# Kernel tuning notes

Measured on AMD Instinct MI355X. Metric: run time of the kernel, lower is better.

## Reference

```python
import jax, jax.numpy as jnp
import numpy as np

CTRL, WORD, MEM, D_IN = 256, 128, 128, 64
B, T = 512, 512
EPS = 1e-6


def setup_inputs() -> dict:
    key = jax.random.key(0)
    ks = jax.random.split(key, 16)
    rs = np.random.RandomState(0)

    data = jax.random.normal(ks[0], (T, B, D_IN), dtype=jnp.float32)

    # ragged lengths -> packed-style batch_sizes (descending, batch_sizes[0]=B)
    lengths = rs.randint(T // 2, T + 1, size=B)
    batch_sizes = jnp.asarray((lengths[None, :] > np.arange(T)[:, None]).sum(1),
                              dtype=jnp.int32)  # [T]
    unsort_idxs = jnp.asarray(rs.permutation(B), dtype=jnp.int32)

    sc = 0.02
    p = lambda k, sh: sc * jax.random.normal(k, sh, dtype=jnp.float32)
    return {
        "data": data,
        "batch_sizes": batch_sizes,
        "unsort_idxs": unsort_idxs,
        # GRU controller: input = D_IN + WORD, hidden = CTRL
        "W_ih": p(ks[1], (3 * CTRL, D_IN + WORD)),
        "b_ih": jnp.zeros((3 * CTRL,), jnp.float32),
        "W_hh": p(ks[2], (3 * CTRL, CTRL)),
        "b_hh": jnp.zeros((3 * CTRL,), jnp.float32),
        # memory head projections (from ctrl_out)
        "W_key": p(ks[3], (WORD, CTRL)), "b_key": jnp.zeros((WORD,), jnp.float32),
        "W_beta": p(ks[4], (1, CTRL)), "b_beta": jnp.zeros((1,), jnp.float32),
        "W_erase": p(ks[5], (WORD, CTRL)), "b_erase": jnp.zeros((WORD,), jnp.float32),
        "W_add": p(ks[6], (WORD, CTRL)), "b_add": jnp.zeros((WORD,), jnp.float32),
        # learned initial memory, shared across batch
        "M0": p(ks[7], (MEM, WORD)),
    }


def _gru(x, h, W_ih, b_ih, W_hh, b_hh):
    gi = x @ W_ih.T + b_ih          # [b, 3*CTRL]
    gh = h @ W_hh.T + b_hh
    ir, iz, inn = jnp.split(gi, 3, axis=-1)
    hr, hz, hn = jnp.split(gh, 3, axis=-1)
    r = jax.nn.sigmoid(ir + hr)
    z = jax.nn.sigmoid(iz + hz)
    n = jnp.tanh(inn + r * hn)
    return (1.0 - z) * n + z * h


def _memory(ctrl, M, W_key, b_key, W_beta, b_beta, W_erase, b_erase, W_add, b_add):
    # content addressing
    k = jnp.tanh(ctrl @ W_key.T + b_key)                       # [b, WORD]
    beta = jax.nn.softplus(ctrl @ W_beta.T + b_beta)           # [b, 1]
    Mn = M / (jnp.linalg.norm(M, axis=-1, keepdims=True) + EPS)
    kn = k / (jnp.linalg.norm(k, axis=-1, keepdims=True) + EPS)
    cos = jnp.einsum('bmw,bw->bm', Mn, kn)                     # [b, MEM]
    w = jax.nn.softmax(beta * cos, axis=-1)                    # [b, MEM]
    read = jnp.einsum('bm,bmw->bw', w, M)                      # [b, WORD]
    # erase/add write
    e = jax.nn.sigmoid(ctrl @ W_erase.T + b_erase)             # [b, WORD]
    a = ctrl @ W_add.T + b_add                                 # [b, WORD]
    M_new = M * (1.0 - w[:, :, None] * e[:, None, :]) + w[:, :, None] * a[:, None, :]
    return read, M_new


def reference(data, batch_sizes, unsort_idxs,
              W_ih, b_ih, W_hh, b_hh,
              W_key, b_key, W_beta, b_beta,
              W_erase, b_erase, W_add, b_add, M0):
    row = jnp.arange(B)

    def step(carry, inp):
        ctrl, read, M = carry
        x_t, size = inp
        active = (row < size)[:, None]                          # [B,1]
        ctrl_in = jnp.concatenate((x_t, read), axis=1)          # [B, D_IN+WORD]
        ctrl_new = _gru(ctrl_in, ctrl, W_ih, b_ih, W_hh, b_hh)
        read_new, M_new = _memory(ctrl_new, M, W_key, b_key, W_beta, b_beta,
                                  W_erase, b_erase, W_add, b_add)
        # inactive rows keep their final state (packed-batch semantics)
        ctrl = jnp.where(active, ctrl_new, ctrl)
        read = jnp.where(active, read_new, read)
        M = jnp.where(active[:, :, None], M_new, M)
        return (ctrl, read, M), None

    init = (jnp.zeros((B, CTRL), data.dtype),
            jnp.zeros((B, WORD), data.dtype),
            jnp.broadcast_to(M0, (B, MEM, WORD)))
    (ctrl, read, _), _ = jax.lax.scan(step, init, (data, batch_sizes))
    return ctrl[unsort_idxs], read[unsort_idxs]
```

## Files before the change

kernel.cpp:

```cpp
#include <hip/hip_runtime.h>
#include <math.h>

#define NB 512
#define NT 512
#define NCTRL 256
#define NWORD 128
#define NMEM 128
#define NDIN 64
#define NACT 448
#define EPSF 1e-6f

#define H_WA   0
#define H_WNI  229376
#define H_WNH  278528
#define H_WH   344064
#define H_TOTAL 475136
#define B_BA   0
#define B_BNI  512
#define B_BNH  768
#define B_BH   1024
#define B_TOTAL 1536
#define WS_BYTES (H_TOTAL * 2 + B_TOTAL * 4)

typedef _Float16 h2 __attribute__((ext_vector_type(2)));
typedef _Float16 h8 __attribute__((ext_vector_type(8)));
union H8 { h8 v; h2 d[4]; };

__device__ __forceinline__ float sigf(float x) { return 1.0f / (1.0f + expf(-x)); }
__device__ __forceinline__ float softplusf(float x) {
    return (x > 15.0f) ? x : log1pf(expf(x));
}
__device__ __forceinline__ float fdot2(h2 a, h2 b, float c) {
#if __has_builtin(__builtin_amdgcn_fdot2)
    return __builtin_amdgcn_fdot2(a, b, c, false);
#else
    return fmaf((float)a[0], (float)b[0], fmaf((float)a[1], (float)b[1], c));
#endif
}

__device__ __forceinline__ void barL() {
    asm volatile("s_waitcnt lgkmcnt(0)\n\ts_barrier" ::: "memory");
}

__global__ __launch_bounds__(256) void prep_kernel(
    const float* __restrict__ Wih, const float* __restrict__ bih,
    const float* __restrict__ Whh, const float* __restrict__ bhh,
    const float* __restrict__ Wkey, const float* __restrict__ bkey,
    const float* __restrict__ Wbeta, const float* __restrict__ bbeta,
    const float* __restrict__ Wer, const float* __restrict__ ber,
    const float* __restrict__ Wadd, const float* __restrict__ badd,
    _Float16* __restrict__ wsH, float* __restrict__ wsB)
{
    int i = blockIdx.x * 256 + threadIdx.x;
    if (i < H_TOTAL) {
        float v;
        if (i < H_WNI) {
            int ch = i >> 3, e = i & 7;
            int kc = ch >> 9, col = ch & 511;
            int k = kc * 8 + e;
            v = (k < 192) ? Wih[col * 192 + k] : Whh[col * 256 + (k - 192)];
        } else if (i < H_WNH) {
            int i2 = i - H_WNI; int ch = i2 >> 3, e = i2 & 7;
            int kc = ch >> 8, col = ch & 255;
            v = Wih[(512 + col) * 192 + kc * 8 + e];
        } else if (i < H_WH) {
            int i2 = i - H_WNH; int ch = i2 >> 3, e = i2 & 7;
            int kc = ch >> 8, col = ch & 255;
            v = Whh[(512 + col) * 256 + kc * 8 + e];
        } else {
            int i2 = i - H_WH; int ch = i2 >> 3, e = i2 & 7;
            int kc = ch >> 9, col = ch & 511;
            int k = kc * 8 + e;
            if (col < 128)       v = Wkey[col * 256 + k];
            else if (col < 256)  v = Wer[(col - 128) * 256 + k];
            else if (col < 384)  v = Wadd[(col - 256) * 256 + k];
            else if (col == 384) v = Wbeta[k];
            else                 v = 0.0f;
        }
        wsH[i] = (_Float16)v;
    } else if (i < H_TOTAL + B_TOTAL) {
        int j = i - H_TOTAL;
        float v;
        if (j < 512)        v = bih[j] + bhh[j];
        else if (j < 768)   v = bih[512 + (j - 512)];
        else if (j < 1024)  v = bhh[512 + (j - 768)];
        else {
            int c = j - 1024;
            if (c < 128)       v = bkey[c];
            else if (c < 256)  v = ber[c - 128];
            else if (c < 384)  v = badd[c - 256];
            else if (c == 384) v = bbeta[0];
            else               v = 0.0f;
        }
        wsB[j] = v;
    }
}

__device__ __forceinline__ void memory_step(
    int u, bool wr, float (*M)[NWORD + 1],
    const float* keyv, const float* ev, const float* av,
    float* cosb, float* wb, float* part, float* readv, float* scal)
{
    if (u < 64) {
        float s = keyv[u] * keyv[u] + keyv[u + 64] * keyv[u + 64];
        #pragma unroll
        for (int o = 32; o >= 1; o >>= 1) s += __shfl_xor(s, o);
        if (u == 0) scal[0] = 1.0f / (sqrtf(s) + EPSF);
    }
    __syncthreads();
    {
        int rr = u >> 1, hh = u & 1;
        const float* Mr = &M[rr][hh * 64];
        const float4* kk4 = (const float4*)(keyv + hh * 64);
        float s2 = 0.f, sc = 0.f;
        #pragma unroll
        for (int p = 0; p < 16; ++p) {
            float4 k4 = kk4[p];
            float m0 = Mr[4 * p], m1 = Mr[4 * p + 1], m2 = Mr[4 * p + 2], m3 = Mr[4 * p + 3];
            s2 = fmaf(m0, m0, s2); sc = fmaf(m0, k4.x, sc);
            s2 = fmaf(m1, m1, s2); sc = fmaf(m1, k4.y, sc);
            s2 = fmaf(m2, m2, s2); sc = fmaf(m2, k4.z, sc);
            s2 = fmaf(m3, m3, s2); sc = fmaf(m3, k4.w, sc);
        }
        s2 += __shfl_xor(s2, 1);
        sc += __shfl_xor(sc, 1);
        if (hh == 0) cosb[rr] = sc * scal[0] / (sqrtf(s2) + EPSF);
    }
    __syncthreads();
    if (u < 64) {
        float beta = scal[1];
        float l0 = beta * cosb[u], l1 = beta * cosb[u + 64];
        float mx = fmaxf(l0, l1);
        #pragma unroll
        for (int o = 32; o >= 1; o >>= 1) mx = fmaxf(mx, __shfl_xor(mx, o));
        float e0 = expf(l0 - mx), e1 = expf(l1 - mx);
        float s = e0 + e1;
        #pragma unroll
        for (int o = 32; o >= 1; o >>= 1) s += __shfl_xor(s, o);
        float inv = 1.0f / s;
        wb[u] = e0 * inv;
        wb[u + 64] = e1 * inv;
    }
    __syncthreads();
    {
        int j = u & 127, rh = u >> 7;
        float ej = ev[j], aj = av[j];
        const float4* wb4 = (const float4*)(wb + rh * 64);
        float p = 0.f;
        #pragma unroll
        for (int pq = 0; pq < 16; ++pq) {
            float4 w4 = wb4[pq];
            int r = rh * 64 + 4 * pq;
            float m0 = M[r][j], m1 = M[r + 1][j], m2 = M[r + 2][j], m3 = M[r + 3][j];
            p = fmaf(w4.x, m0, p);
            p = fmaf(w4.y, m1, p);
            p = fmaf(w4.z, m2, p);
            p = fmaf(w4.w, m3, p);
            if (wr) {
                M[r][j]     = fmaf(-w4.x, fmaf(ej, m0, -aj), m0);
                M[r + 1][j] = fmaf(-w4.y, fmaf(ej, m1, -aj), m1);
                M[r + 2][j] = fmaf(-w4.z, fmaf(ej, m2, -aj), m2);
                M[r + 3][j] = fmaf(-w4.w, fmaf(ej, m3, -aj), m3);
            }
        }
        part[rh * 128 + j] = p;
    }
    __syncthreads();
    if (wr && u < 128) readv[u] = part[u] + part[128 + u];
}

#define DOT_RZ(WSRC) do { H8 w_; w_.v = (WSRC); \
    a0 = fdot2(x0.d[0], w_.d[0], a0); c0 = fdot2(x0.d[1], w_.d[1], c0); \
    a0 = fdot2(x0.d[2], w_.d[2], a0); c0 = fdot2(x0.d[3], w_.d[3], c0); \
    a1 = fdot2(x1.d[0], w_.d[0], a1); c1 = fdot2(x1.d[1], w_.d[1], c1); \
    a1 = fdot2(x1.d[2], w_.d[2], a1); c1 = fdot2(x1.d[3], w_.d[3], c1); } while (0)

#define DOT_AUX(WSRC) do { H8 w_; w_.v = (WSRC); \
    e0 = fdot2(x0.d[0], w_.d[0], e0); f0 = fdot2(x0.d[1], w_.d[1], f0); \
    e0 = fdot2(x0.d[2], w_.d[2], e0); f0 = fdot2(x0.d[3], w_.d[3], f0); \
    e1 = fdot2(x1.d[0], w_.d[0], e1); f1 = fdot2(x1.d[1], w_.d[1], f1); \
    e1 = fdot2(x1.d[2], w_.d[2], e1); f1 = fdot2(x1.d[3], w_.d[3], f1); } while (0)

#define DOT_HD(WSRC) do { H8 w_; w_.v = (WSRC); \
    h0 = fdot2(x0.d[0], w_.d[0], h0); d0 = fdot2(x0.d[1], w_.d[1], d0); \
    h0 = fdot2(x0.d[2], w_.d[2], h0); d0 = fdot2(x0.d[3], w_.d[3], d0); \
    h1 = fdot2(x1.d[0], w_.d[0], h1); d1 = fdot2(x1.d[1], w_.d[1], d1); \
    h1 = fdot2(x1.d[2], w_.d[2], h1); d1 = fdot2(x1.d[3], w_.d[3], d1); } while (0)

#define LOADX(KC) H8 x0; x0.v = A0[KC]; H8 x1; x1.v = A1[KC]

__global__ __launch_bounds__(512) void ntm_fast7(
    const float* __restrict__ data, const int* __restrict__ batch_sizes,
    const int* __restrict__ unsort, const float* __restrict__ M0,
    const _Float16* __restrict__ wsH, const float* __restrict__ wsB,
    float* __restrict__ out)
{
    __shared__ float M[2][NMEM][NWORD + 1];
    __shared__ __align__(16) _Float16 actH[2][NACT];
    __shared__ float ctrlB[2][NCTRL];
    __shared__ float gA[2][512];
    __shared__ float iA[2][NCTRL];
    __shared__ float hA[2][NCTRL];
    __shared__ __align__(16) float readv[2][NWORD], keyv[2][NWORD], ev[2][NWORD], av[2][NWORD];
    __shared__ __align__(16) float cosb[2][NMEM], wb[2][NMEM], part[2][2 * NWORD];
    __shared__ float kn2[2][2], betav[2];
    __shared__ int len_sh[2], gpos[2];

    const int t = threadIdx.x;
    const int q = t >> 8;
    const int u = t & 255;
    const int g = blockIdx.x;
    const int b = 2 * g + q;

    if (t < 2) {
        int bb = 2 * g + t;
        int L = 0;
        for (int s = 0; s < NT; ++s) L += (batch_sizes[s] > bb);
        len_sh[t] = L;
    }
    {
        int ug = unsort[t];
        if (ug == 2 * g)     gpos[0] = t;
        if (ug == 2 * g + 1) gpos[1] = t;
    }
    for (int i = t; i < 2 * NMEM * NWORD; i += 512) {
        int ii = i & (NMEM * NWORD - 1);
        M[i >> 14][ii >> 7][ii & 127] = M0[ii];
    }
    ctrlB[q][u] = 0.0f;
    actH[q][192 + u] = (_Float16)0.0f;
    if (u < NWORD) readv[q][u] = 0.0f;
    __syncthreads();
    const int len0 = len_sh[0], len1 = len_sh[1];

    const float bRZ  = wsB[B_BA + t];
    const float bAux = (t < 256) ? wsB[B_BNI + u] : wsB[B_BNH + u];
    const float bHD  = wsB[B_BH + t];

    const h8* __restrict__ pA  = (const h8*)(wsH + H_WA);
    const h8* __restrict__ pI  = (const h8*)(wsH + H_WNI);
    const h8* __restrict__ pH  = (const h8*)(wsH + H_WNH);
    const h8* __restrict__ pHD = (const h8*)(wsH + H_WH);
    const h8* A0 = (const h8*)actH[0];
    const h8* A1 = (const h8*)actH[1];

    float xf = 0.0f;
    if (u >= 128 && u < 192) xf = data[((long)0 * NB + b) * NDIN + (u - 128)];

    for (int ts = 0; ts < len0; ++ts) {
        const bool wr = (q == 0) | (ts < len1);
        if (u < 128)      actH[q][64 + u] = (_Float16)readv[q][u];
        else if (u < 192) actH[q][u - 128] = (_Float16)xf;
        barL();

        float a0 = bRZ, c0 = 0.f, a1 = bRZ, c1 = 0.f;
        float e0 = bAux, f0 = 0.f, e1 = bAux, f1 = 0.f;
        if (t < 256) {
            #pragma unroll 4
            for (int kc = 0; kc < 24; ++kc) {
                LOADX(kc);
                DOT_RZ(pA[kc * 512 + t]);
                DOT_AUX(pI[kc * 256 + u]);
            }
            #pragma unroll 4
            for (int kc = 24; kc < 56; ++kc) {
                LOADX(kc);
                DOT_RZ(pA[kc * 512 + t]);
            }
        } else {
            #pragma unroll 4
            for (int kc = 0; kc < 24; ++kc) {
                LOADX(kc);
                DOT_RZ(pA[kc * 512 + t]);
            }
            #pragma unroll 4
            for (int kc = 24; kc < 56; ++kc) {
                LOADX(kc);
                DOT_RZ(pA[kc * 512 + t]);
                DOT_AUX(pH[(kc - 24) * 256 + u]);
            }
        }
        gA[0][t] = a0 + c0;
        gA[1][t] = a1 + c1;
        if (t < 256) { iA[0][u] = e0 + f0; iA[1][u] = e1 + f1; }
        else         { hA[0][u] = e0 + f0; hA[1][u] = e1 + f1; }
        barL();

        {
            float rg = sigf(gA[q][u]);
            float zg = sigf(gA[q][NCTRL + u]);
            float ng = tanhf(fmaf(rg, hA[q][u], iA[q][u]));
            float cold = ctrlB[q][u];
            float cnew = fmaf(zg, cold - ng, ng);
            if (wr) {
                ctrlB[q][u] = cnew;
                actH[q][192 + u] = (_Float16)cnew;
            }
        }
        barL();

        {
            float h0 = bHD, d0 = 0.f, h1 = bHD, d1 = 0.f;
            #pragma unroll 4
            for (int kc = 0; kc < 32; ++kc) {
                LOADX(24 + kc);
                DOT_HD(pHD[kc * 512 + t]);
            }
            h0 += d0; h1 += d1;
            if (t < 128) {
                float k0 = tanhf(h0), k1 = tanhf(h1);
                keyv[0][t] = k0; keyv[1][t] = k1;
                float s0 = k0 * k0, s1 = k1 * k1;
                #pragma unroll
                for (int o = 32; o >= 1; o >>= 1) {
                    s0 += __shfl_xor(s0, o);
                    s1 += __shfl_xor(s1, o);
                }
                if ((t & 63) == 0) { kn2[0][t >> 6] = s0; kn2[1][t >> 6] = s1; }
            }
            else if (t < 256)  { ev[0][t - 128] = sigf(h0); ev[1][t - 128] = sigf(h1); }
            else if (t < 384)  { av[0][t - 256] = h0;       av[1][t - 256] = h1; }
            else if (t == 384) { betav[0] = softplusf(h0);  betav[1] = softplusf(h1); }
            int tn = (ts + 1 < NT) ? (ts + 1) : (NT - 1);
            if (u >= 128 && u < 192) xf = data[((long)tn * NB + b) * NDIN + (u - 128)];
        }
        barL();

        {
            float invk = 1.0f / (sqrtf(kn2[q][0] + kn2[q][1]) + EPSF);
            int rr = u >> 1, hh = u & 1;
            const float* Mr = &M[q][rr][hh * 64];
            const float4* kk4 = (const float4*)(&keyv[q][hh * 64]);
            float s2 = 0.f, sc = 0.f;
            #pragma unroll
            for (int p = 0; p < 16; ++p) {
                float4 k4 = kk4[p];
                float m0 = Mr[4 * p], m1 = Mr[4 * p + 1], m2 = Mr[4 * p + 2], m3 = Mr[4 * p + 3];
                s2 = fmaf(m0, m0, s2); sc = fmaf(m0, k4.x, sc);
                s2 = fmaf(m1, m1, s2); sc = fmaf(m1, k4.y, sc);
                s2 = fmaf(m2, m2, s2); sc = fmaf(m2, k4.z, sc);
                s2 = fmaf(m3, m3, s2); sc = fmaf(m3, k4.w, sc);
            }
            s2 += __shfl_xor(s2, 1);
            sc += __shfl_xor(sc, 1);
            if (hh == 0) cosb[q][rr] = sc * invk / (sqrtf(s2) + EPSF);
        }
        barL();

        if (u < 64) {
            float beta = betav[q];
            float l0 = beta * cosb[q][u], l1 = beta * cosb[q][u + 64];
            float mx = fmaxf(l0, l1);
            #pragma unroll
            for (int o = 32; o >= 1; o >>= 1) mx = fmaxf(mx, __shfl_xor(mx, o));
            float se0 = expf(l0 - mx), se1 = expf(l1 - mx);
            float s = se0 + se1;
            #pragma unroll
            for (int o = 32; o >= 1; o >>= 1) s += __shfl_xor(s, o);
            float inv = 1.0f / s;
            wb[q][u] = se0 * inv;
            wb[q][u + 64] = se1 * inv;
        }
        barL();

        {
            int j = u & 127, rh = u >> 7;
            float ej = ev[q][j], aj = av[q][j];
            const float4* wb4 = (const float4*)(&wb[q][rh * 64]);
            float p = 0.f;
            #pragma unroll
            for (int pq = 0; pq < 16; ++pq) {
                float4 w4 = wb4[pq];
                int r = rh * 64 + 4 * pq;
                float m0 = M[q][r][j], m1 = M[q][r + 1][j], m2 = M[q][r + 2][j], m3 = M[q][r + 3][j];
                p = fmaf(w4.x, m0, p);
                p = fmaf(w4.y, m1, p);
                p = fmaf(w4.z, m2, p);
                p = fmaf(w4.w, m3, p);
                if (wr) {
                    M[q][r][j]     = fmaf(-w4.x, fmaf(ej, m0, -aj), m0);
                    M[q][r + 1][j] = fmaf(-w4.y, fmaf(ej, m1, -aj), m1);
                    M[q][r + 2][j] = fmaf(-w4.z, fmaf(ej, m2, -aj), m2);
                    M[q][r + 3][j] = fmaf(-w4.w, fmaf(ej, m3, -aj), m3);
                }
            }
            part[q][rh * 128 + j] = p;
        }
        barL();
        if (wr && u < 128) readv[q][u] = part[q][u] + part[q][128 + u];
    }

    out[gpos[q] * NCTRL + u] = ctrlB[q][u];
    if (u < NWORD) out[NB * NCTRL + gpos[q] * NWORD + u] = readv[q][u];
}

__global__ __launch_bounds__(256) void ntm_slow(
    const float* __restrict__ data, const int* __restrict__ batch_sizes,
    const int* __restrict__ unsort,
    const float* __restrict__ Wih, const float* __restrict__ bih,
    const float* __restrict__ Whh, const float* __restrict__ bhh,
    const float* __restrict__ Wkey, const float* __restrict__ bkey,
    const float* __restrict__ Wbeta, const float* __restrict__ bbeta,
    const float* __restrict__ Wer, const float* __restrict__ ber,
    const float* __restrict__ Wadd, const float* __restrict__ badd,
    const float* __restrict__ M0, float* __restrict__ out)
{
    __shared__ float M[NMEM][NWORD + 1];
    __shared__ float act[NACT];
    __shared__ float ctrlB[NCTRL];
    __shared__ float gpre[512], ginn[256], ghn[256], hpre[448];
    __shared__ __align__(16) float readv[NWORD], keyv[NWORD], ev[NWORD], av[NWORD];
    __shared__ __align__(16) float cosb[NMEM], wb[NMEM], part[2 * NWORD], scal[2];
    __shared__ int len_sh;

    const int tid = threadIdx.x;
    const int g = blockIdx.x;
    const int b = unsort[g];

    if (tid == 0) {
        int L = 0;
        for (int t = 0; t < NT; ++t) L += (batch_sizes[t] > b);
        len_sh = L;
    }
    for (int i = tid; i < NMEM * NWORD; i += 256)
        M[i >> 7][i & 127] = M0[i];
    ctrlB[tid] = 0.0f;
    if (tid < NWORD) readv[tid] = 0.0f;
    __syncthreads();
    const int len = len_sh;
    const int wave = tid >> 6, lane = tid & 63;

    for (int t = 0; t < len; ++t) {
        if (tid < 64)  act[tid] = data[((long)t * NB + b) * NDIN + tid];
        if (tid < 128) act[64 + tid] = readv[tid];
        act[192 + tid] = ctrlB[tid];
        __syncthreads();

        for (int j = wave; j < 512; j += 4) {
            float p = 0.f;
            for (int k = lane; k < 192; k += 64) p = fmaf(act[k], Wih[j * 192 + k], p);
            for (int k = lane; k < 256; k += 64) p = fmaf(act[192 + k], Whh[j * 256 + k], p);
            #pragma unroll
            for (int o = 32; o >= 1; o >>= 1) p += __shfl_xor(p, o);
            if (lane == 0) gpre[j] = p;
        }
        for (int j = wave; j < 256; j += 4) {
            float pi = 0.f, ph = 0.f;
            for (int k = lane; k < 192; k += 64) pi = fmaf(act[k], Wih[(512 + j) * 192 + k], pi);
            for (int k = lane; k < 256; k += 64) ph = fmaf(act[192 + k], Whh[(512 + j) * 256 + k], ph);
            #pragma unroll
            for (int o = 32; o >= 1; o >>= 1) { pi += __shfl_xor(pi, o); ph += __shfl_xor(ph, o); }
            if (lane == 0) { ginn[j] = pi; ghn[j] = ph; }
        }
        __syncthreads();
        {
            float r = sigf(gpre[tid] + bih[tid] + bhh[tid]);
            float z = sigf(gpre[256 + tid] + bih[256 + tid] + bhh[256 + tid]);
            float inn = ginn[tid] + bih[512 + tid];
            float hn  = ghn[tid] + bhh[512 + tid];
            float n = tanhf(fmaf(r, hn, inn));
            float cold = act[192 + tid];
            ctrlB[tid] = fmaf(z, cold - n, n);
        }
        __syncthreads();
        for (int j = wave; j < 385; j += 4) {
            const float* Wp; long base;
            if (j < 128)      { Wp = Wkey;  base = (long)j * 256; }
            else if (j < 256) { Wp = Wer;   base = (long)(j - 128) * 256; }
            else if (j < 384) { Wp = Wadd;  base = (long)(j - 256) * 256; }
            else              { Wp = Wbeta; base = 0; }
            float p = 0.f;
            for (int k = lane; k < 256; k += 64) p = fmaf(ctrlB[k], Wp[base + k], p);
            #pragma unroll
            for (int o = 32; o >= 1; o >>= 1) p += __shfl_xor(p, o);
            if (lane == 0) hpre[j] = p;
        }
        __syncthreads();
        if (tid < 128) {
            keyv[tid] = tanhf(hpre[tid] + bkey[tid]);
            ev[tid]   = sigf(hpre[128 + tid] + ber[tid]);
            av[tid]   = hpre[256 + tid] + badd[tid];
        }
        if (tid == 0) scal[1] = softplusf(hpre[384] + bbeta[0]);
        __syncthreads();

        memory_step(tid, true, M, keyv, ev, av, cosb, wb, part, readv, scal);
        __syncthreads();
    }

    out[g * NCTRL + tid] = ctrlB[tid];
    if (tid < NWORD) out[NB * NCTRL + g * NWORD + tid] = readv[tid];
}

extern "C" void kernel_launch(void* const* d_in, const int* in_sizes, int n_in,
                              void* d_out, int out_size, void* d_ws, size_t ws_size,
                              hipStream_t stream)
{
    const float* data       = (const float*)d_in[0];
    const int*  batch_sizes = (const int*)d_in[1];
    const int*  unsort      = (const int*)d_in[2];
    float* out = (float*)d_out;

    if (ws_size >= (size_t)WS_BYTES) {
        _Float16* wsH = (_Float16*)d_ws;
        float* wsB = (float*)((char*)d_ws + (size_t)H_TOTAL * 2);
        prep_kernel<<<(H_TOTAL + B_TOTAL + 255) / 256, 256, 0, stream>>>(
            (const float*)d_in[3], (const float*)d_in[4], (const float*)d_in[5],
            (const float*)d_in[6], (const float*)d_in[7], (const float*)d_in[8],
            (const float*)d_in[9], (const float*)d_in[10], (const float*)d_in[11],
            (const float*)d_in[12], (const float*)d_in[13], (const float*)d_in[14],
            wsH, wsB);
        ntm_fast7<<<NB / 2, 512, 0, stream>>>(data, batch_sizes, unsort,
                                              (const float*)d_in[15], wsH, wsB, out);
    } else {
        ntm_slow<<<NB, 256, 0, stream>>>(
            data, batch_sizes, unsort,
            (const float*)d_in[3], (const float*)d_in[4], (const float*)d_in[5],
            (const float*)d_in[6], (const float*)d_in[7], (const float*)d_in[8],
            (const float*)d_in[9], (const float*)d_in[10], (const float*)d_in[11],
            (const float*)d_in[12], (const float*)d_in[13], (const float*)d_in[14],
            (const float*)d_in[15], out);
    }
}
```

Before: 6.548 ms.

## Store memory matrix in fp16 shared memory and alias scratch buffers

The per-sample memory matrix moves from fp32 to fp16 in LDS, with a padded row stride. Several per-step scratch arrays now share one union buffer, and the read vector stays in a register instead of shared memory. Together these cut LDS use per block so more blocks fit per CU, with launch bounds asking for 4. In exchange the memory state is quantised to fp16 every step over up to 512 recurrent steps, which risks accuracy drift, and the padded fp16 column accesses may cause bank conflicts.

```diff
diff --git a/kernel.cpp b/kernel.cpp
--- a/kernel.cpp
+++ b/kernel.cpp
@@ -9,6 +9,7 @@
 #define NDIN 64
 #define NACT 448
 #define EPSF 1e-6f
+#define MPAD 130
 
 #define H_WA   0
 #define H_WNI  229376
@@ -189,22 +190,26 @@
 
 #define LOADX(KC) H8 x0; x0.v = A0[KC]; H8 x1; x1.v = A1[KC]
 
-__global__ __launch_bounds__(512) void ntm_fast7(
+__global__ __launch_bounds__(512, 4) void ntm_fast9(
     const float* __restrict__ data, const int* __restrict__ batch_sizes,
     const int* __restrict__ unsort, const float* __restrict__ M0,
     const _Float16* __restrict__ wsH, const float* __restrict__ wsB,
     float* __restrict__ out)
 {
-    __shared__ float M[2][NMEM][NWORD + 1];
+    __shared__ _Float16 Mh[2][NMEM][MPAD];
     __shared__ __align__(16) _Float16 actH[2][NACT];
     __shared__ float ctrlB[2][NCTRL];
-    __shared__ float gA[2][512];
-    __shared__ float iA[2][NCTRL];
-    __shared__ float hA[2][NCTRL];
-    __shared__ __align__(16) float readv[2][NWORD], keyv[2][NWORD], ev[2][NWORD], av[2][NWORD];
-    __shared__ __align__(16) float cosb[2][NMEM], wb[2][NMEM], part[2][2 * NWORD];
+    __shared__ __align__(16) float ubuf[2048];
+    __shared__ __align__(16) float keyv[2][NWORD], ev[2][NWORD], av[2][NWORD];
     __shared__ float kn2[2][2], betav[2];
     __shared__ int len_sh[2], gpos[2];
+
+    float (*gA)[512] = (float (*)[512])(ubuf);
+    float (*iA)[256] = (float (*)[256])(ubuf + 1024);
+    float (*hA)[256] = (float (*)[256])(ubuf + 1536);
+    float (*cosb)[128] = (float (*)[128])(ubuf);
+    float (*wb)[128]   = (float (*)[128])(ubuf + 256);
+    float (*part)[256] = (float (*)[256])(ubuf + 512);
 
     const int t = threadIdx.x;
     const int q = t >> 8;
@@ -225,11 +230,10 @@
     }
     for (int i = t; i < 2 * NMEM * NWORD; i += 512) {
         int ii = i & (NMEM * NWORD - 1);
-        M[i >> 14][ii >> 7][ii & 127] = M0[ii];
+        Mh[i >> 14][ii >> 7][ii & 127] = (_Float16)M0[ii];
     }
     ctrlB[q][u] = 0.0f;
     actH[q][192 + u] = (_Float16)0.0f;
-    if (u < NWORD) readv[q][u] = 0.0f;
     __syncthreads();
     const int len0 = len_sh[0], len1 = len_sh[1];
 
@@ -244,12 +248,13 @@
     const h8* A0 = (const h8*)actH[0];
     const h8* A1 = (const h8*)actH[1];
 
+    float rv = 0.0f;
     float xf = 0.0f;
     if (u >= 128 && u < 192) xf = data[((long)0 * NB + b) * NDIN + (u - 128)];
 
     for (int ts = 0; ts < len0; ++ts) {
         const bool wr = (q == 0) | (ts < len1);
-        if (u < 128)      actH[q][64 + u] = (_Float16)readv[q][u];
+        if (u < 128)      actH[q][64 + u] = (_Float16)rv;
         else if (u < 192) actH[q][u - 128] = (_Float16)xf;
         barL();
 
@@ -329,17 +334,19 @@
         {
             float invk = 1.0f / (sqrtf(kn2[q][0] + kn2[q][1]) + EPSF);
             int rr = u >> 1, hh = u & 1;
-            const float* Mr = &M[q][rr][hh * 64];
+            const h2* Mr2 = (const h2*)&Mh[q][rr][hh * 64];
             const float4* kk4 = (const float4*)(&keyv[q][hh * 64]);
             float s2 = 0.f, sc = 0.f;
             #pragma unroll
             for (int p = 0; p < 16; ++p) {
                 float4 k4 = kk4[p];
-                float m0 = Mr[4 * p], m1 = Mr[4 * p + 1], m2 = Mr[4 * p + 2], m3 = Mr[4 * p + 3];
-                s2 = fmaf(m0, m0, s2); sc = fmaf(m0, k4.x, sc);
-                s2 = fmaf(m1, m1, s2); sc = fmaf(m1, k4.y, sc);
-                s2 = fmaf(m2, m2, s2); sc = fmaf(m2, k4.z, sc);
-                s2 = fmaf(m3, m3, s2); sc = fmaf(m3, k4.w, sc);
+                h2 ma = Mr2[2 * p], mb = Mr2[2 * p + 1];
+                float m0 = (float)ma[0], m1 = (float)ma[1];
+                float m2v = (float)mb[0], m3 = (float)mb[1];
+                s2 = fmaf(m0, m0, s2);   sc = fmaf(m0, k4.x, sc);
+                s2 = fmaf(m1, m1, s2);   sc = fmaf(m1, k4.y, sc);
+                s2 = fmaf(m2v, m2v, s2); sc = fmaf(m2v, k4.z, sc);
+                s2 = fmaf(m3, m3, s2);   sc = fmaf(m3, k4.w, sc);
             }
             s2 += __shfl_xor(s2, 1);
             sc += __shfl_xor(sc, 1);
@@ -372,26 +379,27 @@
             for (int pq = 0; pq < 16; ++pq) {
                 float4 w4 = wb4[pq];
                 int r = rh * 64 + 4 * pq;
-                float m0 = M[q][r][j], m1 = M[q][r + 1][j], m2 = M[q][r + 2][j], m3 = M[q][r + 3][j];
+                float m0 = (float)Mh[q][r][j],     m1 = (float)Mh[q][r + 1][j];
+                float m2v = (float)Mh[q][r + 2][j], m3 = (float)Mh[q][r + 3][j];
                 p = fmaf(w4.x, m0, p);
                 p = fmaf(w4.y, m1, p);
-                p = fmaf(w4.z, m2, p);
+                p = fmaf(w4.z, m2v, p);
                 p = fmaf(w4.w, m3, p);
                 if (wr) {
-                    M[q][r][j]     = fmaf(-w4.x, fmaf(ej, m0, -aj), m0);
-                    M[q][r + 1][j] = fmaf(-w4.y, fmaf(ej, m1, -aj), m1);
-                    M[q][r + 2][j] = fmaf(-w4.z, fmaf(ej, m2, -aj), m2);
-                    M[q][r + 3][j] = fmaf(-w4.w, fmaf(ej, m3, -aj), m3);
+                    Mh[q][r][j]     = (_Float16)fmaf(-w4.x, fmaf(ej, m0, -aj), m0);
+                    Mh[q][r + 1][j] = (_Float16)fmaf(-w4.y, fmaf(ej, m1, -aj), m1);
+                    Mh[q][r + 2][j] = (_Float16)fmaf(-w4.z, fmaf(ej, m2v, -aj), m2v);
+                    Mh[q][r + 3][j] = (_Float16)fmaf(-w4.w, fmaf(ej, m3, -aj), m3);
                 }
             }
             part[q][rh * 128 + j] = p;
         }
         barL();
-        if (wr && u < 128) readv[q][u] = part[q][u] + part[q][128 + u];
+        if (wr && u < 128) rv = part[q][u] + part[q][128 + u];
     }
 
     out[gpos[q] * NCTRL + u] = ctrlB[q][u];
-    if (u < NWORD) out[NB * NCTRL + gpos[q] * NWORD + u] = readv[q][u];
+    if (u < NWORD) out[NB * NCTRL + gpos[q] * NWORD + u] = rv;
 }
 
 __global__ __launch_bounds__(256) void ntm_slow(
@@ -510,7 +518,7 @@
             (const float*)d_in[9], (const float*)d_in[10], (const float*)d_in[11],
             (const float*)d_in[12], (const float*)d_in[13], (const float*)d_in[14],
             wsH, wsB);
-        ntm_fast7<<<NB / 2, 512, 0, stream>>>(data, batch_sizes, unsort,
+        ntm_fast9<<<NB / 2, 512, 0, stream>>>(data, batch_sizes, unsort,
                                               (const float*)d_in[15], wsH, wsB, out);
     } else {
         ntm_slow<<<NB, 256, 0, stream>>>(
```

Result: slower. 8.244 ms (+25.9%).
